# Optimization experiments

Hardware: AMD Instinct MI355X
Metric: run time of the kernel (lower is better)

## Reference

```python
import jax, jax.numpy as jnp
import numpy as np

VOCAB = 50000
EMBED = 512
HIDDEN = 1024
HDIR = HIDDEN // 2  # per-direction LSTM hidden
L = 48              # num_labels
B = 64
T = 512
PAD = 0


def setup_inputs() -> dict:
    key = jax.random.key(0)
    ks = jax.random.split(key, 18)
    def n(k, shape, s=0.05):
        return jax.random.normal(k, shape, jnp.float32) * s
    return {
        "embedding": n(ks[0], (VOCAB, EMBED)),
        "w_ih_f": n(ks[1], (4 * HDIR, EMBED)),
        "w_hh_f": n(ks[2], (4 * HDIR, HDIR)),
        "b_ih_f": n(ks[3], (4 * HDIR,)),
        "b_hh_f": n(ks[4], (4 * HDIR,)),
        "w_ih_b": n(ks[5], (4 * HDIR, EMBED)),
        "w_hh_b": n(ks[6], (4 * HDIR, HDIR)),
        "b_ih_b": n(ks[7], (4 * HDIR,)),
        "b_hh_b": n(ks[8], (4 * HDIR,)),
        "fc_w": n(ks[9], (L, HIDDEN)),
        "fc_b": n(ks[10], (L,)),
        "start_trans": n(ks[11], (L,), 0.1),
        "end_trans": n(ks[12], (L,), 0.1),
        "trans": n(ks[13], (L, L), 0.1),
        "x": jax.random.randint(ks[14], (B, T), 1, VOCAB),   # >=1 so mask all-true
        "tags": jax.random.randint(ks[15], (B, T), 0, L),
    }


def _lstm_dir(emb_tbe, w_ih, w_hh, b_ih, b_hh, reverse):
    # emb_tbe: [T, B, E] -> hs: [T, B, HDIR]; PyTorch gate order i,f,g,o
    Hd = w_hh.shape[1]
    Bb = emb_tbe.shape[1]
    bias = b_ih + b_hh
    def step(carry, x_t):
        h, c = carry
        g = x_t @ w_ih.T + h @ w_hh.T + bias
        i, f, gg, o = jnp.split(g, 4, axis=-1)
        c = jax.nn.sigmoid(f) * c + jax.nn.sigmoid(i) * jnp.tanh(gg)
        h = jax.nn.sigmoid(o) * jnp.tanh(c)
        return (h, c), h
    init = (jnp.zeros((Bb, Hd), emb_tbe.dtype), jnp.zeros((Bb, Hd), emb_tbe.dtype))
    _, hs = jax.lax.scan(step, init, emb_tbe, reverse=reverse)
    return hs


def _crf_nll(emissions_tbl, maskf_tb, tags, start_trans, end_trans, trans):
    # emissions_tbl: [T, B, L]; maskf_tb: [T, B] float; tags: [B, T] int
    em_bt = emissions_tbl.transpose(1, 0, 2)                           # [B, T, L]
    em_tag = jnp.take_along_axis(em_bt, tags[..., None], -1)[..., 0]   # [B, T]
    tr = trans[tags[:, :-1], tags[:, 1:]]                              # [B, T-1]
    mask_bt = maskf_tb.T                                               # [B, T]
    num = start_trans[tags[:, 0]] + em_tag[:, 0] \
        + jnp.sum((em_tag[:, 1:] + tr) * mask_bt[:, 1:], axis=1)
    last_idx = (mask_bt.sum(axis=1) - 1).astype(jnp.int32)
    last_tags = jnp.take_along_axis(tags, last_idx[:, None], 1)[:, 0]
    num = num + end_trans[last_tags]
    # forward algorithm (log partition)
    alpha0 = start_trans[None, :] + emissions_tbl[0]                   # [B, L]
    def step(alpha, inp):
        e_t, m_t = inp
        new = jax.nn.logsumexp(alpha[:, :, None] + trans[None, :, :] + e_t[:, None, :], axis=1)
        return jnp.where(m_t[:, None] > 0, new, alpha), None
    alpha, _ = jax.lax.scan(step, alpha0, (emissions_tbl[1:], maskf_tb[1:]))
    logZ = jax.nn.logsumexp(alpha + end_trans[None, :], axis=-1)       # [B]
    llh = num - logZ
    return -jnp.mean(llh)  # reduction='mean' over batch, negated


def reference(embedding, w_ih_f, w_hh_f, b_ih_f, b_hh_f,
              w_ih_b, w_hh_b, b_ih_b, b_hh_b,
              fc_w, fc_b, start_trans, end_trans, trans, x, tags):
    mask = (x != PAD)                                  # [B, T]
    emb = embedding[x]                                 # [B, T, E]
    emb_t = emb.transpose(1, 0, 2)                     # [T, B, E]
    hf = _lstm_dir(emb_t, w_ih_f, w_hh_f, b_ih_f, b_hh_f, reverse=False)
    hb = _lstm_dir(emb_t, w_ih_b, w_hh_b, b_ih_b, b_hh_b, reverse=True)
    h = jnp.concatenate([hf, hb], axis=-1)             # [T, B, HIDDEN]
    emissions = h @ fc_w.T + fc_b                      # [T, B, L]
    maskf = mask.T.astype(emissions.dtype)             # [T, B]
    return _crf_nll(emissions, maskf, tags, start_trans, end_trans, trans)
```

## Files before the change

### kernel.cpp

```cpp
#include <hip/hip_runtime.h>
#include <hip/hip_bf16.h>


typedef short short8  __attribute__((ext_vector_type(8)));
typedef short short4v __attribute__((ext_vector_type(4)));
typedef float floatx4 __attribute__((ext_vector_type(4)));

#define OFF_XQ    0ULL
#define OFF_H     268435456ULL
#define OFF_EMB   335544320ULL
#define OFF_WIH   369098752ULL
#define OFF_FCW   373293056ULL
#define OFF_BIAS  373391360ULL
#define OFF_EM    373538816ULL
#define OFF_NUM   379830272ULL
#define OFF_LOGZ  379830528ULL
#define WS_NEED   379830784ULL

__device__ __forceinline__ unsigned short f2bf(float f) {
  __hip_bfloat16 h = __float2bfloat16(f);
  unsigned short u; __builtin_memcpy(&u, &h, 2); return u;
}
__device__ __forceinline__ float bf2f(unsigned short u) {
  __hip_bfloat16 h; __builtin_memcpy(&h, &u, 2); return __bfloat162float(h);
}
__device__ __forceinline__ float sigm(float x) { return 1.0f / (1.0f + __expf(-x)); }
__device__ __forceinline__ float tanh_f(float x) {
  x = fmaxf(fminf(x, 15.0f), -15.0f);
  float e = __expf(2.0f * x);
  return (e - 1.0f) / (e + 1.0f);
}
__device__ __forceinline__ int permt(int t) { return (t * 167) & 511; }

__global__ void k_init(uint4* __restrict__ H) {
  size_t i = (size_t)blockIdx.x * 256 + threadIdx.x;
  H[i] = (uint4){0xFFFFFFFFu, 0xFFFFFFFFu, 0xFFFFFFFFu, 0xFFFFFFFFu};
}

__global__ void k0_conv(const float* __restrict__ wf, const float* __restrict__ wb,
                        const float* __restrict__ fcw,
                        const float* __restrict__ bihf, const float* __restrict__ bhhf,
                        const float* __restrict__ bihb, const float* __restrict__ bhhb,
                        unsigned short* __restrict__ wih_bf,
                        unsigned short* __restrict__ fcw_bf,
                        float* __restrict__ bias) {
  int i = blockIdx.x * 256 + threadIdx.x;
  if (i < 1048576) { wih_bf[i] = f2bf(wf[i]); return; }
  int j = i - 1048576;
  if (j < 1048576) { wih_bf[1048576 + j] = f2bf(wb[j]); return; }
  j -= 1048576;
  if (j < 49152) { fcw_bf[j] = f2bf(fcw[j]); return; }
  j -= 49152;
  if (j < 2048) { bias[j] = bihf[j] + bhhf[j]; return; }
  j -= 2048;
  if (j < 2048) { bias[2048 + j] = bihb[j] + bhhb[j]; return; }
}

__global__ void k1_embed(const float* __restrict__ tab, const int* __restrict__ x,
                         unsigned short* __restrict__ emb_bf) {
  int tid = threadIdx.x;
#pragma unroll
  for (int r = 0; r < 4; ++r) {
    int m = blockIdx.x * 4 + r;
    int b = m & 63, t = m >> 6;
    int tok = x[b * 512 + t];
    const float2* src = (const float2*)(tab + (size_t)tok * 512);
    float2 v = src[tid];
    unsigned int pk = (unsigned int)f2bf(v.x) | ((unsigned int)f2bf(v.y) << 16);
    ((unsigned int*)(emb_bf + (size_t)m * 512))[tid] = pk;
  }
}

__global__ __launch_bounds__(256) void k2_xproj(
    const unsigned short* __restrict__ emb_bf, const unsigned short* __restrict__ wih_bf,
    const float* __restrict__ bias, unsigned short* __restrict__ xq) {
  const int mt = blockIdx.x * 128;
  const int nt = blockIdx.y * 128;
  const int d  = blockIdx.z;
  const unsigned short* W = wih_bf + (size_t)d * 2048 * 512;
  __shared__ short Bs[32768];
  const int tid = threadIdx.x, l = tid & 63, wv = tid >> 6;
  const int mh = wv & 1, nh = wv >> 1;
  floatx4 acc[4][4];
#pragma unroll
  for (int a = 0; a < 4; ++a)
#pragma unroll
    for (int b = 0; b < 4; ++b) acc[a][b] = (floatx4){0.f, 0.f, 0.f, 0.f};
  const unsigned short* Abase = emb_bf + (size_t)(mt + mh * 64) * 512;

  for (int kc = 0; kc < 2; ++kc) {
    __syncthreads();
#pragma unroll
    for (int i = 0; i < 16; ++i) {
      int f = i * 4 + wv;
      int nb2 = f & 7, ks = f >> 3;
      int n = nt + nb2 * 16 + (l & 15);
      int k = kc * 256 + ks * 32 + (l >> 4) * 8;
      short8 v = *(const short8*)(W + (size_t)n * 512 + k);
      *(short8*)(Bs + (f * 64 + l) * 8) = v;
    }
    __syncthreads();
#pragma unroll
    for (int ks = 0; ks < 8; ++ks) {
      int k0 = kc * 256 + ks * 32 + (l >> 4) * 8;
      short8 a[4];
#pragma unroll
      for (int mf = 0; mf < 4; ++mf)
        a[mf] = *(const short8*)(Abase + (size_t)(mf * 16 + (l & 15)) * 512 + k0);
#pragma unroll
      for (int nf = 0; nf < 4; ++nf) {
        short8 bfr = *(const short8*)(Bs + ((ks * 8 + nh * 4 + nf) * 64 + l) * 8);
#pragma unroll
        for (int mf = 0; mf < 4; ++mf)
          acc[mf][nf] = __builtin_amdgcn_mfma_f32_16x16x32_bf16(a[mf], bfr, acc[mf][nf], 0, 0, 0);
      }
    }
  }
  __syncthreads();
#pragma unroll
  for (int nf = 0; nf < 4; ++nf) {
    int nl = nh * 64 + nf * 16 + (l & 15);
    float bs = bias[d * 2048 + nt + nl];
#pragma unroll
    for (int mf = 0; mf < 4; ++mf)
#pragma unroll
      for (int r = 0; r < 4; ++r) {
        int ml = mh * 64 + mf * 16 + (l >> 4) * 4 + r;
        Bs[ml * 136 + nl] = (short)f2bf(acc[mf][nf][r] + bs);
      }
  }
  __syncthreads();
  const int chunk = tid >> 3, sub = tid & 7;
  const int g_l = chunk & 15, t_l = chunk >> 4;
  const int gate = nt >> 9, g0 = (nt & 511) >> 3;
  size_t base = (((size_t)(d * 64 + g0 + g_l) * 512) + (size_t)(blockIdx.x * 2 + t_l)) * 2048
                + (size_t)gate * 512 + (size_t)sub * 64;
#pragma unroll
  for (int i = 0; i < 8; ++i) {
    short8 v = *(const short8*)(Bs + (t_l * 64 + sub * 8 + i) * 136 + g_l * 8);
    *(short8*)(xq + base + i * 8) = v;
  }
}

__global__ __launch_bounds__(256, 1) void k3_lstm(
    const float* __restrict__ whh_f, const float* __restrict__ whh_b,
    const unsigned short* __restrict__ xq, unsigned short* __restrict__ Hall) {
  const int wgid = blockIdx.x;
  const int d = wgid >> 6, g = wgid & 63;
  const int tid = threadIdx.x, l = tid & 63, wv = tid >> 6;
  const float* whh = d ? whh_b : whh_f;

  short8 Bf[32];
#pragma unroll
  for (int ks = 0; ks < 16; ++ks) {
#pragma unroll
    for (int T = 0; T < 2; ++T) {
      int nl = l & 15;
      int cA = nl >> 2, gate = nl & 3;
      int row = gate * 512 + g * 8 + 2 * cA + T;
      int k0 = ks * 32 + (l >> 4) * 8;
      const float* src = whh + (size_t)row * 512 + k0;
      short8 v;
#pragma unroll
      for (int j = 0; j < 8; ++j) v[j] = (short)f2bf(src[j]);
      Bf[ks * 2 + T] = v;
    }
  }

  const int q  = l >> 4;
  const int bl = l & 15;
  const int m  = wv * 16 + bl;
  float cst[2] = {0.f, 0.f};

  const unsigned long long* Hb =
      (const unsigned long long*)((const unsigned int*)Hall + (size_t)d * 8388608);
  unsigned int* Hw = (unsigned int*)Hall + (size_t)d * 8388608;
  const unsigned short* xqd = xq + ((size_t)(d * 64 + g) * 512) * 2048;

  const size_t st_dw = (size_t)wv * 4096 + (size_t)(g >> 2) * 256
                     + (size_t)(g & 3) * 64 + bl * 4 + q;

  for (int s = 0; s < 512; ++s) {
    const int t = d ? (511 - s) : s;

    const unsigned int* xb = (const unsigned int*)(xqd + (size_t)t * 2048);
    unsigned int xu[4];
#pragma unroll
    for (int gate = 0; gate < 4; ++gate) xu[gate] = xb[gate * 256 + m * 4 + q];

    floatx4 acc0  = (floatx4){0.f, 0.f, 0.f, 0.f};
    floatx4 acc1  = (floatx4){0.f, 0.f, 0.f, 0.f};
    floatx4 acc0b = (floatx4){0.f, 0.f, 0.f, 0.f};
    floatx4 acc1b = (floatx4){0.f, 0.f, 0.f, 0.f};
    if (s > 0) {
      const int tp = d ? (t + 1) : (t - 1);
      const unsigned long long* Hu = Hb + (size_t)permt(tp) * 8192 + (size_t)wv * 2048;
      unsigned long long u[32];
      for (;;) {
#pragma unroll
        for (int ks = 0; ks < 16; ++ks) {
          u[2 * ks]     = __hip_atomic_load(Hu + (size_t)ks * 128 + 2 * l,
                                            __ATOMIC_RELAXED, __HIP_MEMORY_SCOPE_AGENT);
          u[2 * ks + 1] = __hip_atomic_load(Hu + (size_t)ks * 128 + 2 * l + 1,
                                            __ATOMIC_RELAXED, __HIP_MEMORY_SCOPE_AGENT);
        }
        bool ok = true;
#pragma unroll
        for (int i = 0; i < 32; ++i) {
          ok &= ((unsigned int)u[i] != 0xFFFFFFFFu);
          ok &= ((unsigned int)(u[i] >> 32) != 0xFFFFFFFFu);
        }
        if (__all((int)ok)) break;
        __builtin_amdgcn_s_sleep(1);
      }
#pragma unroll
      for (int ks = 0; ks < 8; ++ks) {
        short8 af0, af1;
        __builtin_memcpy(&af0, &u[2 * ks], 8);
        __builtin_memcpy((char*)&af0 + 8, &u[2 * ks + 1], 8);
        __builtin_memcpy(&af1, &u[2 * (ks + 8)], 8);
        __builtin_memcpy((char*)&af1 + 8, &u[2 * (ks + 8) + 1], 8);
        acc0  = __builtin_amdgcn_mfma_f32_16x16x32_bf16(Bf[ks * 2 + 0], af0, acc0, 0, 0, 0);
        acc1  = __builtin_amdgcn_mfma_f32_16x16x32_bf16(Bf[ks * 2 + 1], af0, acc1, 0, 0, 0);
        acc0b = __builtin_amdgcn_mfma_f32_16x16x32_bf16(Bf[(ks + 8) * 2 + 0], af1, acc0b, 0, 0, 0);
        acc1b = __builtin_amdgcn_mfma_f32_16x16x32_bf16(Bf[(ks + 8) * 2 + 1], af1, acc1b, 0, 0, 0);
      }
      acc0 += acc0b;
      acc1 += acc1b;
    }

    float h2[2];
#pragma unroll
    for (int T = 0; T < 2; ++T) {
      floatx4 a = T ? acc1 : acc0;
      float gi = a[0] + bf2f((unsigned short)(xu[0] >> (16 * T)));
      float gf = a[1] + bf2f((unsigned short)(xu[1] >> (16 * T)));
      float gg = a[2] + bf2f((unsigned short)(xu[2] >> (16 * T)));
      float go = a[3] + bf2f((unsigned short)(xu[3] >> (16 * T)));
      float c = sigm(gf) * cst[T] + sigm(gi) * tanh_f(gg);
      cst[T] = c;
      h2[T] = sigm(go) * tanh_f(c);
    }
    unsigned int hp = (unsigned int)f2bf(h2[0]) | ((unsigned int)f2bf(h2[1]) << 16);
    __hip_atomic_store(&Hw[(size_t)permt(t) * 16384 + st_dw], hp,
                       __ATOMIC_RELAXED, __HIP_MEMORY_SCOPE_AGENT);
    asm volatile("s_waitcnt vmcnt(0)" ::: "memory");
  }
}

__global__ __launch_bounds__(256) void k4_emis(
    const unsigned short* __restrict__ Hall, const unsigned short* __restrict__ fcw_bf,
    const float* __restrict__ fcb, float* __restrict__ em) {
  __shared__ short Fs[48 * 520];
  const int tid = threadIdx.x, l = tid & 63, wv = tid >> 6;
  const int t = blockIdx.x;
  floatx4 acc[3];
  acc[0] = acc[1] = acc[2] = (floatx4){0.f, 0.f, 0.f, 0.f};
  for (int half = 0; half < 2; ++half) {
    __syncthreads();
#pragma unroll
    for (int i = 0; i < 24; ++i) {
      int e4 = (tid + i * 256) * 4;
      int n = e4 >> 9, k = e4 & 511;
      *(short4v*)(Fs + n * 520 + k) =
          *(const short4v*)(fcw_bf + (size_t)n * 1024 + half * 512 + k);
    }
    __syncthreads();
    const unsigned short* Hsrc = Hall + (size_t)half * 16777216 + (size_t)permt(t) * 32768
                                 + (size_t)wv * 8192 + l * 8;
#pragma unroll
    for (int ks = 0; ks < 16; ++ks) {
      short8 a = *(const short8*)(Hsrc + ks * 512);
#pragma unroll
      for (int nf = 0; nf < 3; ++nf) {
        short8 bfr = *(const short8*)(Fs + (nf * 16 + (l & 15)) * 520 + ks * 32 + (l >> 4) * 8);
        acc[nf] = __builtin_amdgcn_mfma_f32_16x16x32_bf16(a, bfr, acc[nf], 0, 0, 0);
      }
    }
  }
#pragma unroll
  for (int nf = 0; nf < 3; ++nf) {
    int n = nf * 16 + (l & 15);
    float bv = fcb[n];
#pragma unroll
    for (int r = 0; r < 4; ++r) {
      int m = wv * 16 + (l >> 4) * 4 + r;
      em[((size_t)t * 64 + m) * 48 + n] = acc[nf][r] + bv;
    }
  }
}

__global__ void k5_num(const float* __restrict__ em, const int* __restrict__ tags,
                       const float* __restrict__ start, const float* __restrict__ endt,
                       const float* __restrict__ trans, float* __restrict__ num) {
  const int b = blockIdx.x, tid = threadIdx.x;
  float s = 0.f;
  for (int t = 1 + tid; t < 512; t += 256) {
    int tg = tags[b * 512 + t], tp = tags[b * 512 + t - 1];
    s += em[(size_t)(t * 64 + b) * 48 + tg] + trans[tp * 48 + tg];
  }
  if (tid == 0) {
    int t0 = tags[b * 512];
    s += start[t0] + em[(size_t)b * 48 + t0] + endt[tags[b * 512 + 511]];
  }
  __shared__ float red[256];
  red[tid] = s;
  __syncthreads();
  for (int o = 128; o > 0; o >>= 1) {
    if (tid < o) red[tid] += red[tid + o];
    __syncthreads();
  }
  if (tid == 0) num[b] = red[0];
}

__global__ void k6_crf(const float* __restrict__ em, const float* __restrict__ trans,
                       const float* __restrict__ start, const float* __restrict__ endt,
                       float* __restrict__ logz) {
  const int b = blockIdx.x;
  const int j = threadIdx.x;
  const bool act = j < 48;
  float Ecol[48];
#pragma unroll
  for (int i = 0; i < 48; ++i) Ecol[i] = act ? __expf(trans[i * 48 + j]) : 0.f;
  __shared__ float p[48];
  float alpha = act ? (start[j] + em[(size_t)b * 48 + j]) : -1e30f;
  for (int t = 1; t < 512; ++t) {
    float e_t = act ? em[(size_t)(t * 64 + b) * 48 + j] : 0.f;
    float m = alpha;
#pragma unroll
    for (int off = 32; off > 0; off >>= 1) m = fmaxf(m, __shfl_xor(m, off));
    if (act) p[j] = __expf(alpha - m);
    float ssum = 0.f;
#pragma unroll
    for (int i = 0; i < 48; ++i) ssum += p[i] * Ecol[i];
    alpha = act ? (m + __logf(ssum) + e_t) : -1e30f;
  }
  float v = act ? (alpha + endt[j]) : -1e30f;
  float m2 = v;
#pragma unroll
  for (int off = 32; off > 0; off >>= 1) m2 = fmaxf(m2, __shfl_xor(m2, off));
  float sz = act ? __expf(v - m2) : 0.f;
#pragma unroll
  for (int off = 32; off > 0; off >>= 1) sz += __shfl_xor(sz, off);
  if (j == 0) logz[b] = m2 + __logf(sz);
}

__global__ void k7_final(const float* __restrict__ num, const float* __restrict__ logz,
                         float* __restrict__ out) {
  int l = threadIdx.x;
  float v = num[l] - logz[l];
#pragma unroll
  for (int off = 32; off > 0; off >>= 1) v += __shfl_xor(v, off);
  if (l == 0) out[0] = -v * (1.0f / 64.0f);
}

extern "C" void kernel_launch(void* const* d_in, const int* in_sizes, int n_in,
                              void* d_out, int out_size, void* d_ws, size_t ws_size,
                              hipStream_t stream) {
  (void)in_sizes; (void)n_in; (void)out_size;
  if (ws_size < WS_NEED) return;

  const float* embedding = (const float*)d_in[0];
  const float* w_ih_f = (const float*)d_in[1];
  const float* w_hh_f = (const float*)d_in[2];
  const float* b_ih_f = (const float*)d_in[3];
  const float* b_hh_f = (const float*)d_in[4];
  const float* w_ih_b = (const float*)d_in[5];
  const float* w_hh_b = (const float*)d_in[6];
  const float* b_ih_b = (const float*)d_in[7];
  const float* b_hh_b = (const float*)d_in[8];
  const float* fc_w = (const float*)d_in[9];
  const float* fc_b = (const float*)d_in[10];
  const float* start_trans = (const float*)d_in[11];
  const float* end_trans = (const float*)d_in[12];
  const float* trans = (const float*)d_in[13];
  const int* x = (const int*)d_in[14];
  const int* tags = (const int*)d_in[15];

  char* ws = (char*)d_ws;
  unsigned short* xq     = (unsigned short*)(ws + OFF_XQ);
  unsigned short* Hall   = (unsigned short*)(ws + OFF_H);
  unsigned short* emb_bf = (unsigned short*)(ws + OFF_EMB);
  unsigned short* wih_bf = (unsigned short*)(ws + OFF_WIH);
  unsigned short* fcw_bf = (unsigned short*)(ws + OFF_FCW);
  float* bias  = (float*)(ws + OFF_BIAS);
  float* em    = (float*)(ws + OFF_EM);
  float* num   = (float*)(ws + OFF_NUM);
  float* logz  = (float*)(ws + OFF_LOGZ);

  k_init<<<16384, 256, 0, stream>>>((uint4*)Hall);
  k0_conv<<<8400, 256, 0, stream>>>(w_ih_f, w_ih_b, fc_w, b_ih_f, b_hh_f, b_ih_b, b_hh_b,
                                    wih_bf, fcw_bf, bias);
  k1_embed<<<8192, 256, 0, stream>>>(embedding, x, emb_bf);
  k2_xproj<<<dim3(256, 16, 2), 256, 0, stream>>>(emb_bf, wih_bf, bias, xq);
  k3_lstm<<<128, 256, 0, stream>>>(w_hh_f, w_hh_b, xq, Hall);
  k4_emis<<<512, 256, 0, stream>>>(Hall, fcw_bf, fc_b, em);
  k5_num<<<64, 256, 0, stream>>>(em, tags, start_trans, end_trans, trans, num);
  k6_crf<<<64, 64, 0, stream>>>(em, trans, start_trans, end_trans, logz);
  k7_final<<<1, 64, 0, stream>>>(num, logz, (float*)d_out);
}
```

Before: 2.688 ms.

## Fuse input projection into LSTM recurrence and overlap it with hidden-state wait

```diff
diff --git a/kernel.cpp b/kernel.cpp
--- a/kernel.cpp
+++ b/kernel.cpp
@@ -41,14 +41,23 @@
                         const float* __restrict__ fcw,
                         const float* __restrict__ bihf, const float* __restrict__ bhhf,
                         const float* __restrict__ bihb, const float* __restrict__ bhhb,
-                        unsigned short* __restrict__ wih_bf,
+                        unsigned short* __restrict__ wfrag,
                         unsigned short* __restrict__ fcw_bf,
                         float* __restrict__ bias) {
   int i = blockIdx.x * 256 + threadIdx.x;
-  if (i < 1048576) { wih_bf[i] = f2bf(wf[i]); return; }
-  int j = i - 1048576;
-  if (j < 1048576) { wih_bf[1048576 + j] = f2bf(wb[j]); return; }
-  j -= 1048576;
+  if (i < 2097152) {
+    int d = i >> 20;
+    int j = i & 1048575;
+    const float* w = d ? wb : wf;
+    int e = j & 7, l = (j >> 3) & 63;
+    int T = (j >> 9) & 1, ks = (j >> 10) & 15, g = j >> 14;
+    int nl = l & 15;
+    int row = (nl & 3) * 512 + g * 8 + 2 * (nl >> 2) + T;
+    int col = ks * 32 + (l >> 4) * 8 + e;
+    wfrag[i] = f2bf(w[(size_t)row * 512 + col]);
+    return;
+  }
+  int j = i - 2097152;
   if (j < 49152) { fcw_bf[j] = f2bf(fcw[j]); return; }
   j -= 49152;
   if (j < 2048) { bias[j] = bihf[j] + bhhf[j]; return; }
@@ -71,80 +80,10 @@
   }
 }
 
-__global__ __launch_bounds__(256) void k2_xproj(
-    const unsigned short* __restrict__ emb_bf, const unsigned short* __restrict__ wih_bf,
-    const float* __restrict__ bias, unsigned short* __restrict__ xq) {
-  const int mt = blockIdx.x * 128;
-  const int nt = blockIdx.y * 128;
-  const int d  = blockIdx.z;
-  const unsigned short* W = wih_bf + (size_t)d * 2048 * 512;
-  __shared__ short Bs[32768];
-  const int tid = threadIdx.x, l = tid & 63, wv = tid >> 6;
-  const int mh = wv & 1, nh = wv >> 1;
-  floatx4 acc[4][4];
-#pragma unroll
-  for (int a = 0; a < 4; ++a)
-#pragma unroll
-    for (int b = 0; b < 4; ++b) acc[a][b] = (floatx4){0.f, 0.f, 0.f, 0.f};
-  const unsigned short* Abase = emb_bf + (size_t)(mt + mh * 64) * 512;
-
-  for (int kc = 0; kc < 2; ++kc) {
-    __syncthreads();
-#pragma unroll
-    for (int i = 0; i < 16; ++i) {
-      int f = i * 4 + wv;
-      int nb2 = f & 7, ks = f >> 3;
-      int n = nt + nb2 * 16 + (l & 15);
-      int k = kc * 256 + ks * 32 + (l >> 4) * 8;
-      short8 v = *(const short8*)(W + (size_t)n * 512 + k);
-      *(short8*)(Bs + (f * 64 + l) * 8) = v;
-    }
-    __syncthreads();
-#pragma unroll
-    for (int ks = 0; ks < 8; ++ks) {
-      int k0 = kc * 256 + ks * 32 + (l >> 4) * 8;
-      short8 a[4];
-#pragma unroll
-      for (int mf = 0; mf < 4; ++mf)
-        a[mf] = *(const short8*)(Abase + (size_t)(mf * 16 + (l & 15)) * 512 + k0);
-#pragma unroll
-      for (int nf = 0; nf < 4; ++nf) {
-        short8 bfr = *(const short8*)(Bs + ((ks * 8 + nh * 4 + nf) * 64 + l) * 8);
-#pragma unroll
-        for (int mf = 0; mf < 4; ++mf)
-          acc[mf][nf] = __builtin_amdgcn_mfma_f32_16x16x32_bf16(a[mf], bfr, acc[mf][nf], 0, 0, 0);
-      }
-    }
-  }
-  __syncthreads();
-#pragma unroll
-  for (int nf = 0; nf < 4; ++nf) {
-    int nl = nh * 64 + nf * 16 + (l & 15);
-    float bs = bias[d * 2048 + nt + nl];
-#pragma unroll
-    for (int mf = 0; mf < 4; ++mf)
-#pragma unroll
-      for (int r = 0; r < 4; ++r) {
-        int ml = mh * 64 + mf * 16 + (l >> 4) * 4 + r;
-        Bs[ml * 136 + nl] = (short)f2bf(acc[mf][nf][r] + bs);
-      }
-  }
-  __syncthreads();
-  const int chunk = tid >> 3, sub = tid & 7;
-  const int g_l = chunk & 15, t_l = chunk >> 4;
-  const int gate = nt >> 9, g0 = (nt & 511) >> 3;
-  size_t base = (((size_t)(d * 64 + g0 + g_l) * 512) + (size_t)(blockIdx.x * 2 + t_l)) * 2048
-                + (size_t)gate * 512 + (size_t)sub * 64;
-#pragma unroll
-  for (int i = 0; i < 8; ++i) {
-    short8 v = *(const short8*)(Bs + (t_l * 64 + sub * 8 + i) * 136 + g_l * 8);
-    *(short8*)(xq + base + i * 8) = v;
-  }
-}
-
 __global__ __launch_bounds__(256, 1) void k3_lstm(
     const float* __restrict__ whh_f, const float* __restrict__ whh_b,
-    const unsigned short* __restrict__ xq, unsigned short* __restrict__ Hall) {
+    const unsigned short* __restrict__ wfrag, const unsigned short* __restrict__ emb_bf,
+    const float* __restrict__ bias, unsigned short* __restrict__ Hall) {
   const int wgid = blockIdx.x;
   const int d = wgid >> 6, g = wgid & 63;
   const int tid = threadIdx.x, l = tid & 63, wv = tid >> 6;
@@ -169,34 +108,69 @@
 
   const int q  = l >> 4;
   const int bl = l & 15;
-  const int m  = wv * 16 + bl;
   float cst[2] = {0.f, 0.f};
+
+  float bs[2][4];
+#pragma unroll
+  for (int T = 0; T < 2; ++T)
+#pragma unroll
+    for (int r = 0; r < 4; ++r)
+      bs[T][r] = bias[d * 2048 + r * 512 + g * 8 + 2 * q + T];
 
   const unsigned long long* Hb =
       (const unsigned long long*)((const unsigned int*)Hall + (size_t)d * 8388608);
   unsigned int* Hw = (unsigned int*)Hall + (size_t)d * 8388608;
-  const unsigned short* xqd = xq + ((size_t)(d * 64 + g) * 512) * 2048;
+  const unsigned short* wfd = wfrag + (size_t)d * 1048576 + (size_t)g * 16384 + l * 8;
 
   const size_t st_dw = (size_t)wv * 4096 + (size_t)(g >> 2) * 256
                      + (size_t)(g & 3) * 64 + bl * 4 + q;
 
   for (int s = 0; s < 512; ++s) {
     const int t = d ? (511 - s) : s;
-
-    const unsigned int* xb = (const unsigned int*)(xqd + (size_t)t * 2048);
-    unsigned int xu[4];
-#pragma unroll
-    for (int gate = 0; gate < 4; ++gate) xu[gate] = xb[gate * 256 + m * 4 + q];
-
+    const int tp = d ? (t + 1) : (t - 1);
+    const unsigned long long* Hu = Hb + (size_t)permt(tp) * 8192 + (size_t)wv * 2048;
+
+    unsigned long long u[32];
+    if (s > 0) {
+#pragma unroll
+      for (int ks = 0; ks < 16; ++ks) {
+        u[2 * ks]     = __hip_atomic_load(Hu + (size_t)ks * 128 + 2 * l,
+                                          __ATOMIC_RELAXED, __HIP_MEMORY_SCOPE_AGENT);
+        u[2 * ks + 1] = __hip_atomic_load(Hu + (size_t)ks * 128 + 2 * l + 1,
+                                          __ATOMIC_RELAXED, __HIP_MEMORY_SCOPE_AGENT);
+      }
+    }
+    __builtin_amdgcn_sched_barrier(0);
+
+    const unsigned short* xbase = emb_bf + ((size_t)(t * 64 + wv * 16 + bl)) * 512 + q * 8;
     floatx4 acc0  = (floatx4){0.f, 0.f, 0.f, 0.f};
     floatx4 acc1  = (floatx4){0.f, 0.f, 0.f, 0.f};
     floatx4 acc0b = (floatx4){0.f, 0.f, 0.f, 0.f};
     floatx4 acc1b = (floatx4){0.f, 0.f, 0.f, 0.f};
+#pragma unroll
+    for (int ks = 0; ks < 8; ++ks) {
+      short8 x0 = *(const short8*)(xbase + ks * 32);
+      short8 x1 = *(const short8*)(xbase + (ks + 8) * 32);
+      short8 w0  = *(const short8*)(wfd + (size_t)(ks * 2 + 0) * 512);
+      short8 w1  = *(const short8*)(wfd + (size_t)(ks * 2 + 1) * 512);
+      short8 w0b = *(const short8*)(wfd + (size_t)((ks + 8) * 2 + 0) * 512);
+      short8 w1b = *(const short8*)(wfd + (size_t)((ks + 8) * 2 + 1) * 512);
+      acc0  = __builtin_amdgcn_mfma_f32_16x16x32_bf16(w0,  x0, acc0,  0, 0, 0);
+      acc1  = __builtin_amdgcn_mfma_f32_16x16x32_bf16(w1,  x0, acc1,  0, 0, 0);
+      acc0b = __builtin_amdgcn_mfma_f32_16x16x32_bf16(w0b, x1, acc0b, 0, 0, 0);
+      acc1b = __builtin_amdgcn_mfma_f32_16x16x32_bf16(w1b, x1, acc1b, 0, 0, 0);
+    }
+
     if (s > 0) {
-      const int tp = d ? (t + 1) : (t - 1);
-      const unsigned long long* Hu = Hb + (size_t)permt(tp) * 8192 + (size_t)wv * 2048;
-      unsigned long long u[32];
       for (;;) {
+        bool ok = true;
+#pragma unroll
+        for (int i = 0; i < 32; ++i) {
+          ok &= ((unsigned int)u[i] != 0xFFFFFFFFu);
+          ok &= ((unsigned int)(u[i] >> 32) != 0xFFFFFFFFu);
+        }
+        if (__all((int)ok)) break;
+        __builtin_amdgcn_s_sleep(1);
 #pragma unroll
         for (int ks = 0; ks < 16; ++ks) {
           u[2 * ks]     = __hip_atomic_load(Hu + (size_t)ks * 128 + 2 * l,
@@ -204,14 +178,6 @@
           u[2 * ks + 1] = __hip_atomic_load(Hu + (size_t)ks * 128 + 2 * l + 1,
                                             __ATOMIC_RELAXED, __HIP_MEMORY_SCOPE_AGENT);
         }
-        bool ok = true;
-#pragma unroll
-        for (int i = 0; i < 32; ++i) {
-          ok &= ((unsigned int)u[i] != 0xFFFFFFFFu);
-          ok &= ((unsigned int)(u[i] >> 32) != 0xFFFFFFFFu);
-        }
-        if (__all((int)ok)) break;
-        __builtin_amdgcn_s_sleep(1);
       }
 #pragma unroll
       for (int ks = 0; ks < 8; ++ks) {
@@ -225,18 +191,18 @@
         acc0b = __builtin_amdgcn_mfma_f32_16x16x32_bf16(Bf[(ks + 8) * 2 + 0], af1, acc0b, 0, 0, 0);
         acc1b = __builtin_amdgcn_mfma_f32_16x16x32_bf16(Bf[(ks + 8) * 2 + 1], af1, acc1b, 0, 0, 0);
       }
-      acc0 += acc0b;
-      acc1 += acc1b;
-    }
+    }
+    acc0 += acc0b;
+    acc1 += acc1b;
 
     float h2[2];
 #pragma unroll
     for (int T = 0; T < 2; ++T) {
       floatx4 a = T ? acc1 : acc0;
-      float gi = a[0] + bf2f((unsigned short)(xu[0] >> (16 * T)));
-      float gf = a[1] + bf2f((unsigned short)(xu[1] >> (16 * T)));
-      float gg = a[2] + bf2f((unsigned short)(xu[2] >> (16 * T)));
-      float go = a[3] + bf2f((unsigned short)(xu[3] >> (16 * T)));
+      float gi = a[0] + bs[T][0];
+      float gf = a[1] + bs[T][1];
+      float gg = a[2] + bs[T][2];
+      float go = a[3] + bs[T][3];
       float c = sigm(gf) * cst[T] + sigm(gi) * tanh_f(gg);
       cst[T] = c;
       h2[T] = sigm(go) * tanh_f(c);
@@ -378,10 +344,9 @@
   const int* tags = (const int*)d_in[15];
 
   char* ws = (char*)d_ws;
-  unsigned short* xq     = (unsigned short*)(ws + OFF_XQ);
   unsigned short* Hall   = (unsigned short*)(ws + OFF_H);
   unsigned short* emb_bf = (unsigned short*)(ws + OFF_EMB);
-  unsigned short* wih_bf = (unsigned short*)(ws + OFF_WIH);
+  unsigned short* wfrag  = (unsigned short*)(ws + OFF_WIH);
   unsigned short* fcw_bf = (unsigned short*)(ws + OFF_FCW);
   float* bias  = (float*)(ws + OFF_BIAS);
   float* em    = (float*)(ws + OFF_EM);
@@ -390,10 +355,9 @@
 
   k_init<<<16384, 256, 0, stream>>>((uint4*)Hall);
   k0_conv<<<8400, 256, 0, stream>>>(w_ih_f, w_ih_b, fc_w, b_ih_f, b_hh_f, b_ih_b, b_hh_b,
-                                    wih_bf, fcw_bf, bias);
+                                    wfrag, fcw_bf, bias);
   k1_embed<<<8192, 256, 0, stream>>>(embedding, x, emb_bf);
-  k2_xproj<<<dim3(256, 16, 2), 256, 0, stream>>>(emb_bf, wih_bf, bias, xq);
-  k3_lstm<<<128, 256, 0, stream>>>(w_hh_f, w_hh_b, xq, Hall);
+  k3_lstm<<<128, 256, 0, stream>>>(w_hh_f, w_hh_b, wfrag, emb_bf, bias, Hall);
   k4_emis<<<512, 256, 0, stream>>>(Hall, fcw_bf, fc_b, em);
   k5_num<<<64, 256, 0, stream>>>(em, tags, start_trans, end_trans, trans, num);
   k6_crf<<<64, 64, 0, stream>>>(em, trans, start_trans, end_trans, logz);
```

After: 3.925 ms. 1.46x slower.
